# Kernel optimization log

Measured on AMD Instinct MI355X. Metric: run time of the kernel, lower is better.

## Reference

```python
import jax, jax.numpy as jnp
import numpy as np

B, S, D, H, DK, DV = 4, 1024, 1024, 16, 64, 64
HALF = D // 2            # 512
DKH = DK // 2            # per-head half q/k dim = 32
DVH = DV // 2            # per-head half v dim = 32


def setup_inputs() -> dict:
    key = jax.random.key(0)
    ks = jax.random.split(key, 12)
    f = lambda k, sh: jax.random.normal(k, sh, dtype=jnp.float32)
    inp = {
        "input_Q": f(ks[0], (B, S, D)),
        "input_K": f(ks[1], (B, S, D)),
        "input_V": f(ks[2], (B, S, D)),
    }
    # causal mask (True = masked), matching attn_mask() helper for non-pad tokens
    causal = jnp.triu(jnp.ones((S, S), dtype=bool), k=1)
    inp["attn_mask"] = jnp.broadcast_to(causal, (B, S, S))
    scale = 0.02
    # projections: [in=HALF, out=DK*H//2=HALF] stored as (in, out) for x @ W
    for i, n in enumerate(["WQ1", "WK1", "WV1", "WQ2", "WK2", "WV2"]):
        inp[n] = f(ks[3 + i], (HALF, DK * H // 2)) * scale
    inp["Wfc1"] = f(ks[9], (H * DV // 2, HALF)) * scale
    inp["Wfc2"] = f(ks[10], (H * DV // 2, HALF)) * scale
    inp["ln_g"] = jnp.ones((HALF,), dtype=jnp.float32)
    inp["ln_b"] = jnp.zeros((HALF,), dtype=jnp.float32)
    return inp


def _layernorm(x, g, b, eps=1e-5):
    mu = jnp.mean(x, axis=-1, keepdims=True)
    var = jnp.mean((x - mu) ** 2, axis=-1, keepdims=True)
    return (x - mu) * jax.lax.rsqrt(var + eps) * g + b


def _heads(x, dh):
    # [B, S, H*dh] -> [B, H, S, dh]
    return x.reshape(B, S, H, dh).transpose(0, 2, 1, 3)


def reference(input_Q, input_K, input_V, attn_mask,
              WQ1, WK1, WV1, WQ2, WK2, WV2, Wfc1, Wfc2, ln_g, ln_b):
    res1 = input_Q[:, :, :HALF]
    res2 = input_Q[:, :, HALF:]
    # half-dim projections, split into heads
    Q1 = _heads(input_Q[:, :, :HALF] @ WQ1, DKH)   # [B,H,S,DKH]
    K1 = _heads(input_K[:, :, :HALF] @ WK1, DKH)
    V1 = _heads(input_V[:, :, :HALF] @ WV1, DVH)
    V2 = _heads(input_V[:, :, HALF:] @ WV2, DVH)
    # Q2/K2 are computed in the original but unused by the attention scores;
    # still compute them for faithfulness (they'd carry grads of zero).
    _Q2 = _heads(input_Q[:, :, HALF:] @ WQ2, DKH)
    _K2 = _heads(input_K[:, :, HALF:] @ WK2, DKH)
    V = jnp.concatenate([V1, V2], axis=-1)         # [B,H,S,DV]
    # attention scores from half-dim Q1/K1 only, scaled by sqrt(d_k//2)
    attn = jnp.einsum("bhqd,bhkd->bhqk", Q1, K1) / np.sqrt(DKH).astype(np.float32)
    masked = jnp.where(attn_mask[:, None, :, :], jnp.float32(-1e9), attn)
    softmax_attn = jax.nn.softmax(masked, axis=-1)  # [B,H,S,S]
    qkv = jnp.einsum("bhqk,bhkd->bhqd", softmax_attn, V)  # [B,H,S,DV]
    qkv_out = qkv.transpose(0, 2, 1, 3).reshape(B, S, H * DV)
    out1 = _layernorm(qkv_out[:, :, : H * DV // 2] @ Wfc1 + res1, ln_g, ln_b)
    out2 = _layernorm(qkv_out[:, :, H * DV // 2 :] @ Wfc2 + res2, ln_g, ln_b)
    output = jnp.concatenate([out1, out2], axis=-1)
    return output, softmax_attn
```

## Files before the change

kernel.cpp:

```cpp
#include <hip/hip_runtime.h>

typedef unsigned short u16;
typedef __attribute__((ext_vector_type(8))) short bf16x8;
typedef __attribute__((ext_vector_type(4))) float f32x4;
typedef __attribute__((ext_vector_type(4))) unsigned short u16x4;

#define B_    4
#define S_    1024
#define D_    1024
#define H_    16
#define BS_   4096
#define HALF_ 512

#define WT_OFF   0
#define QH_OFF   1572864
#define KH_OFF   3670016
#define QKV_OFF  1572864

__device__ __forceinline__ u16 f2b(float f){
    f = (f == f) ? f : 0.f;
    unsigned u; __builtin_memcpy(&u, &f, 4);
    u += 0x7fffu + ((u >> 16) & 1u);
    return (u16)(u >> 16);
}

__global__ __launch_bounds__(256) void k_cvt(
    const float* Q, const float* K, const float* V,
    u16* Qb, u16* Kb, u16* Vb)
{
    const float* src; u16* dst;
    if      (blockIdx.y == 0) { src = Q; dst = Qb; }
    else if (blockIdx.y == 1) { src = K; dst = Kb; }
    else                      { src = V; dst = Vb; }
    size_t i = ((size_t)blockIdx.x * 256 + threadIdx.x) * 4;
    float4 v = *(const float4*)(src + i);
    u16x4 o = { f2b(v.x), f2b(v.y), f2b(v.z), f2b(v.w) };
    *(u16x4*)(dst + i) = o;
}

__global__ __launch_bounds__(256) void k_transpose(
    const float* w0, const float* w1, const float* w2, const float* w3,
    const float* w4, const float* w5, u16* out)
{
    __shared__ u16 tile[32][33];
    const float* src;
    switch (blockIdx.z) {
        case 0: src = w0; break; case 1: src = w1; break; case 2: src = w2; break;
        case 3: src = w3; break; case 4: src = w4; break; default: src = w5; break;
    }
    u16* dst = out + (size_t)blockIdx.z * 512 * 512;
    int tx = threadIdx.x & 31, ty = threadIdx.x >> 5;
    int x = blockIdx.x * 32 + tx;
    #pragma unroll
    for (int j = 0; j < 32; j += 8)
        tile[ty + j][tx] = f2b(src[(size_t)(blockIdx.y * 32 + ty + j) * 512 + x]);
    __syncthreads();
    int x2 = blockIdx.y * 32 + tx;
    #pragma unroll
    for (int j = 0; j < 32; j += 8)
        dst[(size_t)(blockIdx.x * 32 + ty + j) * 512 + x2] = tile[tx][ty + j];
}

__global__ __launch_bounds__(256) void k_proj(
    const u16* Qb, const u16* Kb, const u16* Vb, const u16* WT,
    u16* Qh, u16* Kh, u16* Vh)
{
    int which = blockIdx.z;
    const u16* X; const u16* Wt; int xofs;
    if      (which == 0) { X = Qb; Wt = WT + 0*512*512; xofs = 0;   }
    else if (which == 1) { X = Kb; Wt = WT + 1*512*512; xofs = 0;   }
    else if (which == 2) { X = Vb; Wt = WT + 2*512*512; xofs = 0;   }
    else                 { X = Vb; Wt = WT + 3*512*512; xofs = 512; }

    int lane = threadIdx.x & 63, w = threadIdx.x >> 6;
    int l15 = lane & 15, quad = lane >> 4;
    int m0 = blockIdx.x * 64 + w * 16;
    int n0 = blockIdx.y * 64;

    f32x4 acc[4] = {{0,0,0,0},{0,0,0,0},{0,0,0,0},{0,0,0,0}};
    const u16* arow = X + (size_t)(m0 + l15) * D_ + xofs + quad * 8;

    for (int k0 = 0; k0 < 512; k0 += 32) {
        bf16x8 a = *(const bf16x8*)(arow + k0);
        #pragma unroll
        for (int nt = 0; nt < 4; nt++) {
            bf16x8 b = *(const bf16x8*)(Wt + (size_t)(n0 + nt*16 + l15) * 512 + k0 + quad * 8);
            acc[nt] = __builtin_amdgcn_mfma_f32_16x16x32_bf16(a, b, acc[nt], 0, 0, 0);
        }
    }

    #pragma unroll
    for (int nt = 0; nt < 4; nt++) {
        #pragma unroll
        for (int r = 0; r < 4; r++) {
            int m = m0 + quad * 4 + r;
            int n = n0 + nt * 16 + l15;
            int b = m >> 10, s = m & 1023;
            int h = n >> 5,  d = n & 31;
            u16 v = f2b(acc[nt][r]);
            if (which == 0)      Qh[(((size_t)(b*16 + h))*1024 + s)*32 + d] = v;
            else if (which == 1) Kh[(((size_t)(b*16 + h))*1024 + s)*32 + d] = v;
            else {
                int dofs = (which == 3) ? 32 : 0;
                Vh[(((size_t)(b*16 + h))*1024 + s)*64 + dofs + d] = v;
            }
        }
    }
}

__global__ __launch_bounds__(256) void k_softmax(const u16* Qh, const u16* Kh, float* Pout)
{
    int bh = blockIdx.y;
    int m0 = blockIdx.x * 16;
    int lane = threadIdx.x & 63, w = threadIdx.x >> 6;
    int l15 = lane & 15, quad = lane >> 4;
    __shared__ float red_max[4][16], red_sum[4][16];

    bf16x8 a = *(const bf16x8*)(Qh + ((size_t)bh * 1024 + m0 + l15) * 32 + quad * 8);

    float sc[16][4];
    #pragma unroll
    for (int t = 0; t < 16; t++) {
        int n0 = w * 256 + t * 16;
        if (n0 > m0 + 15) {
            #pragma unroll
            for (int r = 0; r < 4; r++) sc[t][r] = -1e30f;
            continue;
        }
        bf16x8 b = *(const bf16x8*)(Kh + ((size_t)bh * 1024 + n0 + l15) * 32 + quad * 8);
        f32x4 z = {0,0,0,0};
        f32x4 c = __builtin_amdgcn_mfma_f32_16x16x32_bf16(a, b, z, 0, 0, 0);
        int col = n0 + l15;
        #pragma unroll
        for (int r = 0; r < 4; r++) {
            int row = m0 + quad * 4 + r;
            sc[t][r] = (col > row) ? -1e30f : c[r] * 0.17677669529663687f;
        }
    }

    float lmax[4];
    #pragma unroll
    for (int r = 0; r < 4; r++) {
        float m = -1e30f;
        #pragma unroll
        for (int t = 0; t < 16; t++) m = fmaxf(m, sc[t][r]);
        lmax[r] = m;
    }
    #pragma unroll
    for (int mk = 1; mk < 16; mk <<= 1)
        #pragma unroll
        for (int r = 0; r < 4; r++) lmax[r] = fmaxf(lmax[r], __shfl_xor(lmax[r], mk));
    if (l15 == 0)
        #pragma unroll
        for (int r = 0; r < 4; r++) red_max[w][quad * 4 + r] = lmax[r];
    __syncthreads();

    float rmax[4];
    #pragma unroll
    for (int r = 0; r < 4; r++) {
        int row = quad * 4 + r;
        rmax[r] = fmaxf(fmaxf(red_max[0][row], red_max[1][row]),
                        fmaxf(red_max[2][row], red_max[3][row]));
    }

    float lsum[4] = {0, 0, 0, 0};
    #pragma unroll
    for (int t = 0; t < 16; t++)
        #pragma unroll
        for (int r = 0; r < 4; r++) {
            float e = (sc[t][r] <= -1e29f) ? 0.f : __expf(sc[t][r] - rmax[r]);
            sc[t][r] = e; lsum[r] += e;
        }
    #pragma unroll
    for (int mk = 1; mk < 16; mk <<= 1)
        #pragma unroll
        for (int r = 0; r < 4; r++) lsum[r] += __shfl_xor(lsum[r], mk);
    if (l15 == 0)
        #pragma unroll
        for (int r = 0; r < 4; r++) red_sum[w][quad * 4 + r] = lsum[r];
    __syncthreads();

    #pragma unroll
    for (int r = 0; r < 4; r++) {
        int row = quad * 4 + r;
        float tot = red_sum[0][row] + red_sum[1][row] + red_sum[2][row] + red_sum[3][row];
        float inv = (tot > 0.f) ? 1.f / tot : 0.f;
        size_t rowbase = ((size_t)bh * 1024 + m0 + row) * 1024 + w * 256 + l15;
        #pragma unroll
        for (int t = 0; t < 16; t++)
            Pout[rowbase + t * 16] = sc[t][r] * inv;
    }
}

__global__ __launch_bounds__(256) void k_pv(const float* P, const u16* Vh, u16* QKV)
{
    int bh = blockIdx.y;
    int m0 = blockIdx.x * 64;
    int lane = threadIdx.x & 63, w = threadIdx.x >> 6;
    int l15 = lane & 15, quad = lane >> 4;
    __shared__ u16 vt[64][72];

    f32x4 acc[4] = {{0,0,0,0},{0,0,0,0},{0,0,0,0},{0,0,0,0}};
    int nchunks = blockIdx.x + 1;
    const float* prow = P + ((size_t)bh * 1024 + m0 + w * 16 + l15) * 1024 + quad * 8;

    for (int c = 0; c < nchunks; c++) {
        int k0 = c * 64;
        int kk = threadIdx.x >> 2, dv0 = (threadIdx.x & 3) * 16;
        const u16* vsrc = Vh + ((size_t)bh * 1024 + k0 + kk) * 64 + dv0;
        bf16x8 v0 = *(const bf16x8*)(vsrc);
        bf16x8 v1 = *(const bf16x8*)(vsrc + 8);
        __syncthreads();
        #pragma unroll
        for (int i = 0; i < 8; i++) vt[dv0 + i][kk]     = (u16)v0[i];
        #pragma unroll
        for (int i = 0; i < 8; i++) vt[dv0 + 8 + i][kk] = (u16)v1[i];
        __syncthreads();

        #pragma unroll
        for (int ks = 0; ks < 2; ks++) {
            float4 pa = *(const float4*)(prow + k0 + ks * 32);
            float4 pb = *(const float4*)(prow + k0 + ks * 32 + 4);
            bf16x8 a;
            a[0] = (short)f2b(pa.x); a[1] = (short)f2b(pa.y);
            a[2] = (short)f2b(pa.z); a[3] = (short)f2b(pa.w);
            a[4] = (short)f2b(pb.x); a[5] = (short)f2b(pb.y);
            a[6] = (short)f2b(pb.z); a[7] = (short)f2b(pb.w);
            #pragma unroll
            for (int nt = 0; nt < 4; nt++) {
                bf16x8 b = *(const bf16x8*)(&vt[nt * 16 + l15][ks * 32 + quad * 8]);
                acc[nt] = __builtin_amdgcn_mfma_f32_16x16x32_bf16(a, b, acc[nt], 0, 0, 0);
            }
        }
    }

    int b = bh >> 4, h = bh & 15;
    #pragma unroll
    for (int nt = 0; nt < 4; nt++)
        #pragma unroll
        for (int r = 0; r < 4; r++) {
            int s  = m0 + w * 16 + quad * 4 + r;
            int dv = nt * 16 + l15;
            QKV[((size_t)b * 1024 + s) * 1024 + h * 64 + dv] = f2b(acc[nt][r]);
        }
}

__global__ __launch_bounds__(256) void k_fc(
    const u16* QKV, const u16* WT, const float* resQ,
    const float* lng, const float* lnb, float* out)
{
    int half = blockIdx.y;
    int m0 = blockIdx.x * 16;
    int lane = threadIdx.x & 63, w = threadIdx.x >> 6;
    int l15 = lane & 15, quad = lane >> 4;
    __shared__ float red_s[4][16], red_q[4][16];

    const u16* Wt = WT + (size_t)(4 + half) * 512 * 512;
    f32x4 acc[8] = {{0,0,0,0},{0,0,0,0},{0,0,0,0},{0,0,0,0},
                    {0,0,0,0},{0,0,0,0},{0,0,0,0},{0,0,0,0}};
    const u16* arow = QKV + (size_t)(m0 + l15) * 1024 + half * 512 + quad * 8;

    for (int k0 = 0; k0 < 512; k0 += 32) {
        bf16x8 a = *(const bf16x8*)(arow + k0);
        #pragma unroll
        for (int f = 0; f < 8; f++) {
            int n = w * 128 + f * 16 + l15;
            bf16x8 b = *(const bf16x8*)(Wt + (size_t)n * 512 + k0 + quad * 8);
            acc[f] = __builtin_amdgcn_mfma_f32_16x16x32_bf16(a, b, acc[f], 0, 0, 0);
        }
    }

    #pragma unroll
    for (int f = 0; f < 8; f++)
        #pragma unroll
        for (int r = 0; r < 4; r++) {
            int row = m0 + quad * 4 + r;
            int col = w * 128 + f * 16 + l15;
            acc[f][r] += resQ[(size_t)row * 1024 + half * 512 + col];
        }

    float psum[4] = {0,0,0,0}, psq[4] = {0,0,0,0};
    #pragma unroll
    for (int f = 0; f < 8; f++)
        #pragma unroll
        for (int r = 0; r < 4; r++) { psum[r] += acc[f][r]; psq[r] += acc[f][r] * acc[f][r]; }
    #pragma unroll
    for (int mk = 1; mk < 16; mk <<= 1)
        #pragma unroll
        for (int r = 0; r < 4; r++) {
            psum[r] += __shfl_xor(psum[r], mk);
            psq[r]  += __shfl_xor(psq[r],  mk);
        }
    if (l15 == 0)
        #pragma unroll
        for (int r = 0; r < 4; r++) { red_s[w][quad*4+r] = psum[r]; red_q[w][quad*4+r] = psq[r]; }
    __syncthreads();

    #pragma unroll
    for (int r = 0; r < 4; r++) {
        int row = quad * 4 + r;
        float s  = red_s[0][row] + red_s[1][row] + red_s[2][row] + red_s[3][row];
        float q  = red_q[0][row] + red_q[1][row] + red_q[2][row] + red_q[3][row];
        float mu = s * (1.f / 512.f);
        float var = fmaxf(q * (1.f / 512.f) - mu * mu, 0.f);
        float rstd = rsqrtf(var + 1e-5f);
        #pragma unroll
        for (int f = 0; f < 8; f++) {
            int col = w * 128 + f * 16 + l15;
            float g = lng[col], bb = lnb[col];
            float v = (acc[f][r] - mu) * rstd * g + bb;
            out[(size_t)(m0 + row) * 1024 + half * 512 + col] = v;
        }
    }
}

extern "C" void kernel_launch(void* const* d_in, const int* in_sizes, int n_in,
                              void* d_out, int out_size, void* d_ws, size_t ws_size,
                              hipStream_t stream)
{
    const float* Q    = (const float*)d_in[0];
    const float* K    = (const float*)d_in[1];
    const float* V    = (const float*)d_in[2];
    const float* WQ1  = (const float*)d_in[4];
    const float* WK1  = (const float*)d_in[5];
    const float* WV1  = (const float*)d_in[6];
    const float* WV2  = (const float*)d_in[9];
    const float* Wfc1 = (const float*)d_in[10];
    const float* Wfc2 = (const float*)d_in[11];
    const float* lng  = (const float*)d_in[12];
    const float* lnb  = (const float*)d_in[13];

    float* out  = (float*)d_out;
    u16*   ws   = (u16*)d_ws;
    u16*   WT   = ws + WT_OFF;
    u16*   Qh   = ws + QH_OFF;
    u16*   Kh   = ws + KH_OFF;
    u16*   QKV  = ws + QKV_OFF;
    u16*   Vh   = (u16*)d_out;
    float* attn = out + (size_t)BS_ * D_;
    u16*   Qb   = (u16*)attn;
    u16*   Kb   = Qb + (size_t)BS_ * D_;
    u16*   Vb   = Kb + (size_t)BS_ * D_;

    k_cvt      <<<dim3(4096, 3),   256, 0, stream>>>(Q, K, V, Qb, Kb, Vb);
    k_transpose<<<dim3(16, 16, 6), 256, 0, stream>>>(WQ1, WK1, WV1, WV2, Wfc1, Wfc2, WT);
    k_proj     <<<dim3(64, 8, 4),  256, 0, stream>>>(Qb, Kb, Vb, WT, Qh, Kh, Vh);
    k_softmax  <<<dim3(64, 64),    256, 0, stream>>>(Qh, Kh, attn);
    k_pv       <<<dim3(16, 64),    256, 0, stream>>>(attn, Vh, QKV);
    k_fc       <<<dim3(256, 2),    256, 0, stream>>>(QKV, WT, Q, lng, lnb, out);
}
```

Baseline: 559.4 us.

## Fuse input conversion into projection, transpose V, stage softmax stores, widen fc tiles

Drops the separate fp32-to-bf16 conversion kernel and converts Q/K/V on the fly inside the projection GEMM. V is now stored pre-transposed, so the PV kernel reads MFMA B operands straight from global memory with no LDS transpose or barriers. The softmax kernel stages probabilities in shared memory so each row is written with coalesced float4 stores. Softmax and PV also launch the heaviest causal row blocks first, and the fc+layernorm kernel handles 32 rows per block to reuse each weight load twice. The trade-offs are larger LDS use in softmax, which may lower occupancy, a strided scatter when writing transposed V, and removal of the NaN guard in the bf16 conversion.

```diff
diff --git a/kernel.cpp b/kernel.cpp
--- a/kernel.cpp
+++ b/kernel.cpp
@@ -3,7 +3,6 @@
 typedef unsigned short u16;
 typedef __attribute__((ext_vector_type(8))) short bf16x8;
 typedef __attribute__((ext_vector_type(4))) float f32x4;
-typedef __attribute__((ext_vector_type(4))) unsigned short u16x4;
 
 #define B_    4
 #define S_    1024
@@ -18,24 +17,15 @@
 #define QKV_OFF  1572864
 
 __device__ __forceinline__ u16 f2b(float f){
-    f = (f == f) ? f : 0.f;
     unsigned u; __builtin_memcpy(&u, &f, 4);
     u += 0x7fffu + ((u >> 16) & 1u);
     return (u16)(u >> 16);
 }
-
-__global__ __launch_bounds__(256) void k_cvt(
-    const float* Q, const float* K, const float* V,
-    u16* Qb, u16* Kb, u16* Vb)
-{
-    const float* src; u16* dst;
-    if      (blockIdx.y == 0) { src = Q; dst = Qb; }
-    else if (blockIdx.y == 1) { src = K; dst = Kb; }
-    else                      { src = V; dst = Vb; }
-    size_t i = ((size_t)blockIdx.x * 256 + threadIdx.x) * 4;
-    float4 v = *(const float4*)(src + i);
-    u16x4 o = { f2b(v.x), f2b(v.y), f2b(v.z), f2b(v.w) };
-    *(u16x4*)(dst + i) = o;
+__device__ __forceinline__ bf16x8 pack8(float4 a, float4 b){
+    bf16x8 r;
+    r[0] = (short)f2b(a.x); r[1] = (short)f2b(a.y); r[2] = (short)f2b(a.z); r[3] = (short)f2b(a.w);
+    r[4] = (short)f2b(b.x); r[5] = (short)f2b(b.y); r[6] = (short)f2b(b.z); r[7] = (short)f2b(b.w);
+    return r;
 }
 
 __global__ __launch_bounds__(256) void k_transpose(
@@ -62,15 +52,15 @@
 }
 
 __global__ __launch_bounds__(256) void k_proj(
-    const u16* Qb, const u16* Kb, const u16* Vb, const u16* WT,
-    u16* Qh, u16* Kh, u16* Vh)
+    const float* Q, const float* K, const float* V, const u16* WT,
+    u16* Qh, u16* Kh, u16* Vt)
 {
     int which = blockIdx.z;
-    const u16* X; const u16* Wt; int xofs;
-    if      (which == 0) { X = Qb; Wt = WT + 0*512*512; xofs = 0;   }
-    else if (which == 1) { X = Kb; Wt = WT + 1*512*512; xofs = 0;   }
-    else if (which == 2) { X = Vb; Wt = WT + 2*512*512; xofs = 0;   }
-    else                 { X = Vb; Wt = WT + 3*512*512; xofs = 512; }
+    const float* X; const u16* Wt; int xofs;
+    if      (which == 0) { X = Q; Wt = WT + 0*512*512; xofs = 0;   }
+    else if (which == 1) { X = K; Wt = WT + 1*512*512; xofs = 0;   }
+    else if (which == 2) { X = V; Wt = WT + 2*512*512; xofs = 0;   }
+    else                 { X = V; Wt = WT + 3*512*512; xofs = 512; }
 
     int lane = threadIdx.x & 63, w = threadIdx.x >> 6;
     int l15 = lane & 15, quad = lane >> 4;
@@ -78,10 +68,12 @@
     int n0 = blockIdx.y * 64;
 
     f32x4 acc[4] = {{0,0,0,0},{0,0,0,0},{0,0,0,0},{0,0,0,0}};
-    const u16* arow = X + (size_t)(m0 + l15) * D_ + xofs + quad * 8;
+    const float* arow = X + (size_t)(m0 + l15) * D_ + xofs + quad * 8;
 
     for (int k0 = 0; k0 < 512; k0 += 32) {
-        bf16x8 a = *(const bf16x8*)(arow + k0);
+        float4 fa = *(const float4*)(arow + k0);
+        float4 fbv = *(const float4*)(arow + k0 + 4);
+        bf16x8 a = pack8(fa, fbv);
         #pragma unroll
         for (int nt = 0; nt < 4; nt++) {
             bf16x8 b = *(const bf16x8*)(Wt + (size_t)(n0 + nt*16 + l15) * 512 + k0 + quad * 8);
@@ -97,12 +89,13 @@
             int n = n0 + nt * 16 + l15;
             int b = m >> 10, s = m & 1023;
             int h = n >> 5,  d = n & 31;
+            int bh = b * 16 + h;
             u16 v = f2b(acc[nt][r]);
-            if (which == 0)      Qh[(((size_t)(b*16 + h))*1024 + s)*32 + d] = v;
-            else if (which == 1) Kh[(((size_t)(b*16 + h))*1024 + s)*32 + d] = v;
+            if (which == 0)      Qh[((size_t)bh * 1024 + s) * 32 + d] = v;
+            else if (which == 1) Kh[((size_t)bh * 1024 + s) * 32 + d] = v;
             else {
-                int dofs = (which == 3) ? 32 : 0;
-                Vh[(((size_t)(b*16 + h))*1024 + s)*64 + dofs + d] = v;
+                int dv = (which == 3) ? 32 + d : d;
+                Vt[((size_t)bh * 64 + dv) * 1024 + s] = v;
             }
         }
     }
@@ -111,10 +104,11 @@
 __global__ __launch_bounds__(256) void k_softmax(const u16* Qh, const u16* Kh, float* Pout)
 {
     int bh = blockIdx.y;
-    int m0 = blockIdx.x * 16;
+    int m0 = (63 - blockIdx.x) * 16;
     int lane = threadIdx.x & 63, w = threadIdx.x >> 6;
     int l15 = lane & 15, quad = lane >> 4;
     __shared__ float red_max[4][16], red_sum[4][16];
+    __shared__ float pbuf[4][16][276];
 
     bf16x8 a = *(const bf16x8*)(Qh + ((size_t)bh * 1024 + m0 + l15) * 32 + quad * 8);
 
@@ -185,52 +179,40 @@
         int row = quad * 4 + r;
         float tot = red_sum[0][row] + red_sum[1][row] + red_sum[2][row] + red_sum[3][row];
         float inv = (tot > 0.f) ? 1.f / tot : 0.f;
-        size_t rowbase = ((size_t)bh * 1024 + m0 + row) * 1024 + w * 256 + l15;
         #pragma unroll
         for (int t = 0; t < 16; t++)
-            Pout[rowbase + t * 16] = sc[t][r] * inv;
-    }
-}
-
-__global__ __launch_bounds__(256) void k_pv(const float* P, const u16* Vh, u16* QKV)
+            pbuf[w][row][t * 16 + l15] = sc[t][r] * inv;
+    }
+    __syncthreads();
+
+    size_t base = ((size_t)bh * 1024 + m0) * 1024 + w * 256;
+    #pragma unroll
+    for (int row = 0; row < 16; row++) {
+        float4 v = *(const float4*)&pbuf[w][row][lane * 4];
+        *(float4*)(Pout + base + (size_t)row * 1024 + lane * 4) = v;
+    }
+}
+
+__global__ __launch_bounds__(256) void k_pv(const float* P, const u16* Vt, u16* QKV)
 {
     int bh = blockIdx.y;
-    int m0 = blockIdx.x * 64;
+    int m0 = (int)(gridDim.x - 1 - blockIdx.x) * 64;
     int lane = threadIdx.x & 63, w = threadIdx.x >> 6;
     int l15 = lane & 15, quad = lane >> 4;
-    __shared__ u16 vt[64][72];
 
     f32x4 acc[4] = {{0,0,0,0},{0,0,0,0},{0,0,0,0},{0,0,0,0}};
-    int nchunks = blockIdx.x + 1;
+    int kmax = m0 + 64;
     const float* prow = P + ((size_t)bh * 1024 + m0 + w * 16 + l15) * 1024 + quad * 8;
-
-    for (int c = 0; c < nchunks; c++) {
-        int k0 = c * 64;
-        int kk = threadIdx.x >> 2, dv0 = (threadIdx.x & 3) * 16;
-        const u16* vsrc = Vh + ((size_t)bh * 1024 + k0 + kk) * 64 + dv0;
-        bf16x8 v0 = *(const bf16x8*)(vsrc);
-        bf16x8 v1 = *(const bf16x8*)(vsrc + 8);
-        __syncthreads();
-        #pragma unroll
-        for (int i = 0; i < 8; i++) vt[dv0 + i][kk]     = (u16)v0[i];
-        #pragma unroll
-        for (int i = 0; i < 8; i++) vt[dv0 + 8 + i][kk] = (u16)v1[i];
-        __syncthreads();
-
-        #pragma unroll
-        for (int ks = 0; ks < 2; ks++) {
-            float4 pa = *(const float4*)(prow + k0 + ks * 32);
-            float4 pb = *(const float4*)(prow + k0 + ks * 32 + 4);
-            bf16x8 a;
-            a[0] = (short)f2b(pa.x); a[1] = (short)f2b(pa.y);
-            a[2] = (short)f2b(pa.z); a[3] = (short)f2b(pa.w);
-            a[4] = (short)f2b(pb.x); a[5] = (short)f2b(pb.y);
-            a[6] = (short)f2b(pb.z); a[7] = (short)f2b(pb.w);
-            #pragma unroll
-            for (int nt = 0; nt < 4; nt++) {
-                bf16x8 b = *(const bf16x8*)(&vt[nt * 16 + l15][ks * 32 + quad * 8]);
-                acc[nt] = __builtin_amdgcn_mfma_f32_16x16x32_bf16(a, b, acc[nt], 0, 0, 0);
-            }
+    const u16*   vrow = Vt + ((size_t)bh * 64 + l15) * 1024 + quad * 8;
+
+    for (int k0 = 0; k0 < kmax; k0 += 32) {
+        float4 pa = *(const float4*)(prow + k0);
+        float4 pb = *(const float4*)(prow + k0 + 4);
+        bf16x8 a = pack8(pa, pb);
+        #pragma unroll
+        for (int nt = 0; nt < 4; nt++) {
+            bf16x8 b = *(const bf16x8*)(vrow + (size_t)nt * 16 * 1024 + k0);
+            acc[nt] = __builtin_amdgcn_mfma_f32_16x16x32_bf16(a, b, acc[nt], 0, 0, 0);
         }
     }
 
@@ -250,68 +232,80 @@
     const float* lng, const float* lnb, float* out)
 {
     int half = blockIdx.y;
-    int m0 = blockIdx.x * 16;
+    int m0 = blockIdx.x * 32;
     int lane = threadIdx.x & 63, w = threadIdx.x >> 6;
     int l15 = lane & 15, quad = lane >> 4;
-    __shared__ float red_s[4][16], red_q[4][16];
+    __shared__ float red_s[2][4][16], red_q[2][4][16];
 
     const u16* Wt = WT + (size_t)(4 + half) * 512 * 512;
-    f32x4 acc[8] = {{0,0,0,0},{0,0,0,0},{0,0,0,0},{0,0,0,0},
-                    {0,0,0,0},{0,0,0,0},{0,0,0,0},{0,0,0,0}};
-    const u16* arow = QKV + (size_t)(m0 + l15) * 1024 + half * 512 + quad * 8;
+    f32x4 acc[2][8];
+    #pragma unroll
+    for (int mt = 0; mt < 2; mt++)
+        #pragma unroll
+        for (int f = 0; f < 8; f++) acc[mt][f] = (f32x4){0,0,0,0};
+
+    const u16* arow0 = QKV + (size_t)(m0 + l15) * 1024 + half * 512 + quad * 8;
+    const u16* arow1 = arow0 + (size_t)16 * 1024;
 
     for (int k0 = 0; k0 < 512; k0 += 32) {
-        bf16x8 a = *(const bf16x8*)(arow + k0);
+        bf16x8 a0 = *(const bf16x8*)(arow0 + k0);
+        bf16x8 a1 = *(const bf16x8*)(arow1 + k0);
         #pragma unroll
         for (int f = 0; f < 8; f++) {
             int n = w * 128 + f * 16 + l15;
             bf16x8 b = *(const bf16x8*)(Wt + (size_t)n * 512 + k0 + quad * 8);
-            acc[f] = __builtin_amdgcn_mfma_f32_16x16x32_bf16(a, b, acc[f], 0, 0, 0);
-        }
-    }
-
-    #pragma unroll
-    for (int f = 0; f < 8; f++)
-        #pragma unroll
-        for (int r = 0; r < 4; r++) {
-            int row = m0 + quad * 4 + r;
-            int col = w * 128 + f * 16 + l15;
-            acc[f][r] += resQ[(size_t)row * 1024 + half * 512 + col];
-        }
-
-    float psum[4] = {0,0,0,0}, psq[4] = {0,0,0,0};
-    #pragma unroll
-    for (int f = 0; f < 8; f++)
-        #pragma unroll
-        for (int r = 0; r < 4; r++) { psum[r] += acc[f][r]; psq[r] += acc[f][r] * acc[f][r]; }
-    #pragma unroll
-    for (int mk = 1; mk < 16; mk <<= 1)
-        #pragma unroll
-        for (int r = 0; r < 4; r++) {
-            psum[r] += __shfl_xor(psum[r], mk);
-            psq[r]  += __shfl_xor(psq[r],  mk);
-        }
-    if (l15 == 0)
-        #pragma unroll
-        for (int r = 0; r < 4; r++) { red_s[w][quad*4+r] = psum[r]; red_q[w][quad*4+r] = psq[r]; }
-    __syncthreads();
-
-    #pragma unroll
-    for (int r = 0; r < 4; r++) {
-        int row = quad * 4 + r;
-        float s  = red_s[0][row] + red_s[1][row] + red_s[2][row] + red_s[3][row];
-        float q  = red_q[0][row] + red_q[1][row] + red_q[2][row] + red_q[3][row];
-        float mu = s * (1.f / 512.f);
-        float var = fmaxf(q * (1.f / 512.f) - mu * mu, 0.f);
-        float rstd = rsqrtf(var + 1e-5f);
-        #pragma unroll
-        for (int f = 0; f < 8; f++) {
-            int col = w * 128 + f * 16 + l15;
-            float g = lng[col], bb = lnb[col];
-            float v = (acc[f][r] - mu) * rstd * g + bb;
-            out[(size_t)(m0 + row) * 1024 + half * 512 + col] = v;
-        }
-    }
+            acc[0][f] = __builtin_amdgcn_mfma_f32_16x16x32_bf16(a0, b, acc[0][f], 0, 0, 0);
+            acc[1][f] = __builtin_amdgcn_mfma_f32_16x16x32_bf16(a1, b, acc[1][f], 0, 0, 0);
+        }
+    }
+
+    #pragma unroll
+    for (int mt = 0; mt < 2; mt++) {
+        float psum[4] = {0,0,0,0}, psq[4] = {0,0,0,0};
+        #pragma unroll
+        for (int f = 0; f < 8; f++)
+            #pragma unroll
+            for (int r = 0; r < 4; r++) {
+                int row = m0 + mt * 16 + quad * 4 + r;
+                int col = w * 128 + f * 16 + l15;
+                float v = acc[mt][f][r] + resQ[(size_t)row * 1024 + half * 512 + col];
+                acc[mt][f][r] = v;
+                psum[r] += v; psq[r] += v * v;
+            }
+        #pragma unroll
+        for (int mk = 1; mk < 16; mk <<= 1)
+            #pragma unroll
+            for (int r = 0; r < 4; r++) {
+                psum[r] += __shfl_xor(psum[r], mk);
+                psq[r]  += __shfl_xor(psq[r],  mk);
+            }
+        if (l15 == 0)
+            #pragma unroll
+            for (int r = 0; r < 4; r++) {
+                red_s[mt][w][quad*4+r] = psum[r];
+                red_q[mt][w][quad*4+r] = psq[r];
+            }
+    }
+    __syncthreads();
+
+    #pragma unroll
+    for (int mt = 0; mt < 2; mt++)
+        #pragma unroll
+        for (int r = 0; r < 4; r++) {
+            int row = quad * 4 + r;
+            float s  = red_s[mt][0][row] + red_s[mt][1][row] + red_s[mt][2][row] + red_s[mt][3][row];
+            float q  = red_q[mt][0][row] + red_q[mt][1][row] + red_q[mt][2][row] + red_q[mt][3][row];
+            float mu = s * (1.f / 512.f);
+            float var = fmaxf(q * (1.f / 512.f) - mu * mu, 0.f);
+            float rstd = rsqrtf(var + 1e-5f);
+            #pragma unroll
+            for (int f = 0; f < 8; f++) {
+                int col = w * 128 + f * 16 + l15;
+                float g = lng[col], bb = lnb[col];
+                float v = (acc[mt][f][r] - mu) * rstd * g + bb;
+                out[(size_t)(m0 + mt * 16 + row) * 1024 + half * 512 + col] = v;
+            }
+        }
 }
 
 extern "C" void kernel_launch(void* const* d_in, const int* in_sizes, int n_in,
@@ -336,16 +330,12 @@
     u16*   Qh   = ws + QH_OFF;
     u16*   Kh   = ws + KH_OFF;
     u16*   QKV  = ws + QKV_OFF;
-    u16*   Vh   = (u16*)d_out;
+    u16*   Vt   = (u16*)d_out;
     float* attn = out + (size_t)BS_ * D_;
-    u16*   Qb   = (u16*)attn;
-    u16*   Kb   = Qb + (size_t)BS_ * D_;
-    u16*   Vb   = Kb + (size_t)BS_ * D_;
-
-    k_cvt      <<<dim3(4096, 3),   256, 0, stream>>>(Q, K, V, Qb, Kb, Vb);
+
     k_transpose<<<dim3(16, 16, 6), 256, 0, stream>>>(WQ1, WK1, WV1, WV2, Wfc1, Wfc2, WT);
-    k_proj     <<<dim3(64, 8, 4),  256, 0, stream>>>(Qb, Kb, Vb, WT, Qh, Kh, Vh);
+    k_proj     <<<dim3(64, 8, 4),  256, 0, stream>>>(Q, K, V, WT, Qh, Kh, Vt);
     k_softmax  <<<dim3(64, 64),    256, 0, stream>>>(Qh, Kh, attn);
-    k_pv       <<<dim3(16, 64),    256, 0, stream>>>(attn, Vh, QKV);
-    k_fc       <<<dim3(256, 2),    256, 0, stream>>>(QKV, WT, Q, lng, lnb, out);
-}
+    k_pv       <<<dim3(16, 64),    256, 0, stream>>>(attn, Vt, QKV);
+    k_fc       <<<dim3(128, 2),    256, 0, stream>>>(QKV, WT, Q, lng, lnb, out);
+}
```

After: 601.3 us. 1.08x slower.
